# Kernel tuning notes

Measured on AMD Instinct MI355X. Metric: run time of the kernel, lower is better.

Reference implementation:

```python
import jax, jax.numpy as jnp
import numpy as np

B, H, W, D, K = 32, 64, 64, 128, 1024

def setup_inputs() -> dict:
    key = jax.random.key(0)
    k1, k2 = jax.random.split(key)
    inputs = jax.random.normal(k1, (B, H, W, D), dtype=jnp.float32)
    embedding = jax.random.normal(k2, (D, K), dtype=jnp.float32)  # codebook, column per code
    return {"inputs": inputs, "embedding": embedding}

def reference(inputs, embedding):
    D_ = embedding.shape[0]
    x = inputs.reshape(-1, D_)                                  # [N, D]
    dist = (jnp.sum(x * x, axis=-1, keepdims=True)
            - 2.0 * (x @ embedding)
            + jnp.sum(embedding * embedding, axis=0, keepdims=True))  # [N, K]
    idx = jnp.argmax(-dist, axis=1).reshape(inputs.shape[:-1])  # [B, H, W]
    return embedding.T[idx]                                     # [B, H, W, D]
```

## Files before the change

### kernel.cpp

```cpp
#include <hip/hip_runtime.h>

#define KC 1024
#define DD 128
#define NT_COUNT (KC / 16)

typedef short bf16x8 __attribute__((ext_vector_type(8)));
typedef float f32x4  __attribute__((ext_vector_type(4)));

#define AS1 __attribute__((address_space(1)))
#define AS3 __attribute__((address_space(3)))

static __device__ __forceinline__ unsigned short f2bf(float f) {
    unsigned u = __float_as_uint(f);
    unsigned r = (u + 0x7fffu + ((u >> 16) & 1u)) >> 16;
    return (unsigned short)r;
}
static __device__ __forceinline__ float bf2f(unsigned short h) {
    return __uint_as_float(((unsigned)h) << 16);
}
static __device__ __forceinline__ void gl_lds16(const void* g, void* l) {
    __builtin_amdgcn_global_load_lds((const AS1 void*)g, (AS3 void*)l, 16, 0, 0);
}
static __device__ __forceinline__ void gl_lds4(const void* g, void* l) {
    __builtin_amdgcn_global_load_lds((const AS1 void*)g, (AS3 void*)l, 4, 0, 0);
}

__global__ __launch_bounds__(256) void vq_prep(const float* __restrict__ E,
                                               float* __restrict__ e2h,
                                               float* __restrict__ ET,
                                               unsigned short* __restrict__ Bpk) {
    __shared__ float T[16 * 129];
    const int nt  = blockIdx.x;
    const int tid = threadIdx.x;

    for (int i = tid; i < 16 * DD; i += 256) {
        int d  = i >> 4;
        int kk = i & 15;
        T[kk * 129 + d] = E[(size_t)d * KC + nt * 16 + kk];
    }
    __syncthreads();

    if (tid < 16) {
        float s = 0.f;
#pragma unroll 16
        for (int d = 0; d < DD; ++d) {
            float v = T[tid * 129 + d];
            s = fmaf(v, v, s);
        }
        e2h[nt * 16 + tid] = 512.0f - 0.5f * s;
    }

    for (int i = tid; i < 16 * DD; i += 256) {
        int kk = i >> 7;
        int d  = i & 127;
        ET[(size_t)(nt * 16 + kk) * DD + d] = T[kk * 129 + d];
    }

    {
        const int s    = tid >> 6;
        const int lane = tid & 63;
        const int kk   = lane & 15;
        const int d0   = s * 32 + (lane >> 4) * 8;
        bf16x8 hi, lo;
#pragma unroll
        for (int j = 0; j < 8; ++j) {
            float v = T[kk * 129 + d0 + j];
            unsigned short h = f2bf(v);
            hi[j] = (short)h;
            lo[j] = (short)f2bf(v - bf2f(h));
        }
        char* base = (char*)Bpk + (size_t)nt * 8192 + s * 1024 + lane * 16;
        *(bf16x8*)(base)        = hi;
        *(bf16x8*)(base + 4096) = lo;
    }
}

__global__ __launch_bounds__(64, 3) void vq_main(const float* __restrict__ X,
                                                 const float* __restrict__ e2h,
                                                 const float* __restrict__ ET,
                                                 const unsigned short* __restrict__ Bpk,
                                                 float* __restrict__ Out) {
    __shared__ __align__(16) char lds[16896];
    int*    s_k1  = (int*)(lds);
    int*    s_k2  = (int*)(lds + 128);
    int*    s_win = (int*)(lds + 256);
    double* s_d   = (double*)(lds + 384);

    const int lane  = threadIdx.x;
    const int quad  = lane >> 4;
    const int n16   = lane & 15;
    const int wrow0 = blockIdx.x * 32;

    bf16x8 ahi[2][4], alo[2][4];
#pragma unroll
    for (int t = 0; t < 2; ++t) {
#pragma unroll
        for (int s = 0; s < 4; ++s) {
            const int row = wrow0 + t * 16 + n16;
            const int d0  = s * 32 + quad * 8;
            const float4 p = *(const float4*)(X + (size_t)row * DD + d0);
            const float4 q = *(const float4*)(X + (size_t)row * DD + d0 + 4);
            float v[8] = {p.x, p.y, p.z, p.w, q.x, q.y, q.z, q.w};
#pragma unroll
            for (int j = 0; j < 8; ++j) {
                unsigned short h = f2bf(v[j]);
                ahi[t][s][j] = (short)h;
                alo[t][s][j] = (short)f2bf(v[j] - bf2f(h));
            }
        }
    }

    float p1[2][4], p2[2][4];
#pragma unroll
    for (int t = 0; t < 2; ++t)
#pragma unroll
        for (int r = 0; r < 4; ++r) { p1[t][r] = 0.0f; p2[t][r] = 0.0f; }

    const char* gB = (const char*)Bpk + (size_t)lane * 16;

    auto stage = [&](int nt, int buf) {
        const char* g = gB + (size_t)nt * 8192;
        char* l = lds + buf * 8192;
#pragma unroll
        for (int c = 0; c < 8; ++c)
            gl_lds16(g + c * 1024, l + c * 1024);
        gl_lds4(e2h + nt * 16 + n16, lds + 16384 + buf * 256);
    };

    stage(0, 0);

    for (int nt = 0; nt < NT_COUNT; ++nt) {
        const int cur = nt & 1;
        if (nt + 1 < NT_COUNT) {
            stage(nt + 1, cur ^ 1);
            __builtin_amdgcn_s_waitcnt(3961);
        } else {
            __builtin_amdgcn_s_waitcnt(3952);
        }
        __builtin_amdgcn_sched_barrier(0);

        const char* l = lds + cur * 8192;
        const bf16x8 bh0 = *(const bf16x8*)(l + 0 * 1024 + lane * 16);
        const bf16x8 bh1 = *(const bf16x8*)(l + 1 * 1024 + lane * 16);
        const bf16x8 bh2 = *(const bf16x8*)(l + 2 * 1024 + lane * 16);
        const bf16x8 bh3 = *(const bf16x8*)(l + 3 * 1024 + lane * 16);
        const bf16x8 bl0 = *(const bf16x8*)(l + 4 * 1024 + lane * 16);
        const bf16x8 bl1 = *(const bf16x8*)(l + 5 * 1024 + lane * 16);
        const bf16x8 bl2 = *(const bf16x8*)(l + 6 * 1024 + lane * 16);
        const bf16x8 bl3 = *(const bf16x8*)(l + 7 * 1024 + lane * 16);
        const float  ev  = *(const float*)(lds + 16384 + cur * 256 + lane * 4);
        const unsigned ntinv = (unsigned)(63 - nt);

#pragma unroll
        for (int t = 0; t < 2; ++t) {
            f32x4 acc = {ev, ev, ev, ev};
            acc = __builtin_amdgcn_mfma_f32_16x16x32_bf16(ahi[t][0], bh0, acc, 0, 0, 0);
            acc = __builtin_amdgcn_mfma_f32_16x16x32_bf16(ahi[t][1], bh1, acc, 0, 0, 0);
            acc = __builtin_amdgcn_mfma_f32_16x16x32_bf16(ahi[t][2], bh2, acc, 0, 0, 0);
            acc = __builtin_amdgcn_mfma_f32_16x16x32_bf16(ahi[t][3], bh3, acc, 0, 0, 0);
            acc = __builtin_amdgcn_mfma_f32_16x16x32_bf16(alo[t][0], bh0, acc, 0, 0, 0);
            acc = __builtin_amdgcn_mfma_f32_16x16x32_bf16(alo[t][1], bh1, acc, 0, 0, 0);
            acc = __builtin_amdgcn_mfma_f32_16x16x32_bf16(alo[t][2], bh2, acc, 0, 0, 0);
            acc = __builtin_amdgcn_mfma_f32_16x16x32_bf16(alo[t][3], bh3, acc, 0, 0, 0);
            acc = __builtin_amdgcn_mfma_f32_16x16x32_bf16(ahi[t][0], bl0, acc, 0, 0, 0);
            acc = __builtin_amdgcn_mfma_f32_16x16x32_bf16(ahi[t][1], bl1, acc, 0, 0, 0);
            acc = __builtin_amdgcn_mfma_f32_16x16x32_bf16(ahi[t][2], bl2, acc, 0, 0, 0);
            acc = __builtin_amdgcn_mfma_f32_16x16x32_bf16(ahi[t][3], bl3, acc, 0, 0, 0);
#pragma unroll
            for (int r = 0; r < 4; ++r) {
                float v = __uint_as_float((__float_as_uint(acc[r]) & ~63u) | ntinv);
                float lo = fminf(p1[t][r], v);
                p1[t][r] = fmaxf(p1[t][r], v);
                p2[t][r] = fmaxf(p2[t][r], lo);
            }
        }
    }
    __syncthreads();

#pragma unroll
    for (int t = 0; t < 2; ++t) {
#pragma unroll
        for (int r = 0; r < 4; ++r) {
            unsigned u1 = __float_as_uint(p1[t][r]);
            unsigned u2 = __float_as_uint(p2[t][r]);
            int k1 = (int)(63u - (u1 & 63u)) * 16 + n16;
            int k2 = (int)(63u - (u2 & 63u)) * 16 + n16;
            unsigned long long q1 =
                ((unsigned long long)(u1 & ~63u) << 32) | (unsigned)(1023 - k1);
            unsigned long long q2 =
                ((unsigned long long)(u2 & ~63u) << 32) | (unsigned)(1023 - k2);
#pragma unroll
            for (int m = 1; m < 16; m <<= 1) {
                unsigned long long o1 = __shfl_xor(q1, m, 64);
                unsigned long long o2 = __shfl_xor(q2, m, 64);
                unsigned long long lo = q1 < o1 ? q1 : o1;
                q1 = q1 > o1 ? q1 : o1;
                unsigned long long hi2 = q2 > o2 ? q2 : o2;
                q2 = lo > hi2 ? lo : hi2;
            }
            if (n16 == 0) {
                int row = t * 16 + quad * 4 + r;
                s_k1[row] = 1023 - (int)(q1 & 1023u);
                s_k2[row] = 1023 - (int)(q2 & 1023u);
            }
        }
    }
    __syncthreads();

    {
        const int row = lane >> 1;
        const int k   = (lane & 1) ? s_k2[row] : s_k1[row];
        const float* __restrict__ xrow = X + (size_t)(wrow0 + row) * DD;
        const float* __restrict__ erow = ET + (size_t)k * DD;
        double dot = 0.0, ee = 0.0;
#pragma unroll 8
        for (int d = 0; d < DD; ++d) {
            double xv = (double)xrow[d];
            double evd = (double)erow[d];
            dot = fma(xv, evd, dot);
            ee  = fma(evd, evd, ee);
        }
        s_d[lane] = ee - 2.0 * dot;
    }
    __syncthreads();
    if (lane < 32) {
        double d1 = s_d[2 * lane];
        double d2 = s_d[2 * lane + 1];
        int kk1 = s_k1[lane], kk2 = s_k2[lane];
        s_win[lane] = (d2 < d1 || (d2 == d1 && kk2 < kk1)) ? kk2 : kk1;
    }
    __syncthreads();

    for (int i = lane; i < 32 * (DD / 4); i += 64) {
        const int row = i >> 5;
        const int d4  = i & 31;
        const float4 v = *(const float4*)(ET + (size_t)s_win[row] * DD + d4 * 4);
        *(float4*)(Out + (size_t)(wrow0 + row) * DD + d4 * 4) = v;
    }
}

extern "C" void kernel_launch(void* const* d_in, const int* in_sizes, int n_in,
                              void* d_out, int out_size, void* d_ws, size_t ws_size,
                              hipStream_t stream) {
    const float* X = (const float*)d_in[0];
    const float* E = (const float*)d_in[1];
    float* Out = (float*)d_out;

    float* e2h = (float*)d_ws;
    float* ET  = e2h + KC;
    unsigned short* Bpk = (unsigned short*)(ET + (size_t)KC * DD);

    const int N = in_sizes[0] / DD;

    hipLaunchKernelGGL(vq_prep, dim3(NT_COUNT), dim3(256), 0, stream, E, e2h, ET, Bpk);
    hipLaunchKernelGGL(vq_main, dim3(N / 32), dim3(64), 0, stream,
                       X, e2h, ET, Bpk, Out);
}
```

Before: 249.0 us.

## Double rows per wave to halve codebook LDS traffic and unroll pipeline by two

Each single-wave block now handles 64 rows (4 MFMA row tiles) instead of 32, so every staged codebook tile is reused across twice as many rows. This halves the total codebook global-to-LDS traffic and the number of blocks. The double-buffered loop is manually unrolled by two with fixed buffer offsets, and the exact fp64 rerank now has one lane per row checking both candidates. The cost is roughly double the register use for A fragments and accumulators, occupancy hint lowered from 3 to 2, and fewer blocks for load balance.

```diff
diff --git a/kernel.cpp b/kernel.cpp
--- a/kernel.cpp
+++ b/kernel.cpp
@@ -3,6 +3,7 @@
 #define KC 1024
 #define DD 128
 #define NT_COUNT (KC / 16)
+#define RPB 64
 
 typedef short bf16x8 __attribute__((ext_vector_type(8)));
 typedef float f32x4  __attribute__((ext_vector_type(4)));
@@ -75,25 +76,26 @@
     }
 }
 
-__global__ __launch_bounds__(64, 3) void vq_main(const float* __restrict__ X,
+__global__ __launch_bounds__(64, 2) void vq_main(const float* __restrict__ X,
                                                  const float* __restrict__ e2h,
                                                  const float* __restrict__ ET,
                                                  const unsigned short* __restrict__ Bpk,
                                                  float* __restrict__ Out) {
-    __shared__ __align__(16) char lds[16896];
-    int*    s_k1  = (int*)(lds);
-    int*    s_k2  = (int*)(lds + 128);
-    int*    s_win = (int*)(lds + 256);
-    double* s_d   = (double*)(lds + 384);
+    __shared__ __align__(16) char lds[2 * 8448];
+    int* s_k1  = (int*)(lds);
+    int* s_k2  = (int*)(lds + 256);
+    int* s_win = (int*)(lds + 512);
 
     const int lane  = threadIdx.x;
     const int quad  = lane >> 4;
     const int n16   = lane & 15;
-    const int wrow0 = blockIdx.x * 32;
-
-    bf16x8 ahi[2][4], alo[2][4];
-#pragma unroll
-    for (int t = 0; t < 2; ++t) {
+    const int wrow0 = blockIdx.x * RPB;
+    const int lidx16 = lane * 16;
+    const int lidx4  = lane * 4;
+
+    bf16x8 ahi[4][4], alo[4][4];
+#pragma unroll
+    for (int t = 0; t < 4; ++t) {
 #pragma unroll
         for (int s = 0; s < 4; ++s) {
             const int row = wrow0 + t * 16 + n16;
@@ -110,75 +112,79 @@
         }
     }
 
-    float p1[2][4], p2[2][4];
-#pragma unroll
-    for (int t = 0; t < 2; ++t)
+    float p1[4][4], p2[4][4];
+#pragma unroll
+    for (int t = 0; t < 4; ++t)
 #pragma unroll
         for (int r = 0; r < 4; ++r) { p1[t][r] = 0.0f; p2[t][r] = 0.0f; }
 
-    const char* gB = (const char*)Bpk + (size_t)lane * 16;
-
-    auto stage = [&](int nt, int buf) {
-        const char* g = gB + (size_t)nt * 8192;
-        char* l = lds + buf * 8192;
-#pragma unroll
-        for (int c = 0; c < 8; ++c)
-            gl_lds16(g + c * 1024, l + c * 1024);
-        gl_lds4(e2h + nt * 16 + n16, lds + 16384 + buf * 256);
-    };
-
-    stage(0, 0);
-
-    for (int nt = 0; nt < NT_COUNT; ++nt) {
-        const int cur = nt & 1;
-        if (nt + 1 < NT_COUNT) {
-            stage(nt + 1, cur ^ 1);
+#define STAGE(NT, BOFF)                                                          \
+    do {                                                                         \
+        const char* g = (const char*)Bpk + (size_t)(NT) * 8192;                  \
+        _Pragma("unroll")                                                        \
+        for (int c = 0; c < 8; ++c)                                              \
+            gl_lds16(g + c * 1024 + lidx16, lds + (BOFF) + c * 1024);            \
+        gl_lds4(e2h + (NT) * 16 + n16, lds + (BOFF) + 8192);                     \
+    } while (0)
+
+#define TILE(NT, BOFF)                                                           \
+    do {                                                                         \
+        const char* l = lds + (BOFF);                                            \
+        const bf16x8 bh0 = *(const bf16x8*)(l + 0 * 1024 + lidx16);              \
+        const bf16x8 bh1 = *(const bf16x8*)(l + 1 * 1024 + lidx16);              \
+        const bf16x8 bh2 = *(const bf16x8*)(l + 2 * 1024 + lidx16);              \
+        const bf16x8 bh3 = *(const bf16x8*)(l + 3 * 1024 + lidx16);              \
+        const bf16x8 bl0 = *(const bf16x8*)(l + 4 * 1024 + lidx16);              \
+        const bf16x8 bl1 = *(const bf16x8*)(l + 5 * 1024 + lidx16);              \
+        const bf16x8 bl2 = *(const bf16x8*)(l + 6 * 1024 + lidx16);              \
+        const bf16x8 bl3 = *(const bf16x8*)(l + 7 * 1024 + lidx16);              \
+        const float  ev  = *(const float*)(l + 8192 + lidx4);                    \
+        const unsigned ntinv = (unsigned)(63 - (NT));                            \
+        _Pragma("unroll")                                                        \
+        for (int t = 0; t < 4; ++t) {                                            \
+            f32x4 acc = {ev, ev, ev, ev};                                        \
+            acc = __builtin_amdgcn_mfma_f32_16x16x32_bf16(ahi[t][0], bh0, acc, 0, 0, 0); \
+            acc = __builtin_amdgcn_mfma_f32_16x16x32_bf16(ahi[t][1], bh1, acc, 0, 0, 0); \
+            acc = __builtin_amdgcn_mfma_f32_16x16x32_bf16(ahi[t][2], bh2, acc, 0, 0, 0); \
+            acc = __builtin_amdgcn_mfma_f32_16x16x32_bf16(ahi[t][3], bh3, acc, 0, 0, 0); \
+            acc = __builtin_amdgcn_mfma_f32_16x16x32_bf16(alo[t][0], bh0, acc, 0, 0, 0); \
+            acc = __builtin_amdgcn_mfma_f32_16x16x32_bf16(alo[t][1], bh1, acc, 0, 0, 0); \
+            acc = __builtin_amdgcn_mfma_f32_16x16x32_bf16(alo[t][2], bh2, acc, 0, 0, 0); \
+            acc = __builtin_amdgcn_mfma_f32_16x16x32_bf16(alo[t][3], bh3, acc, 0, 0, 0); \
+            acc = __builtin_amdgcn_mfma_f32_16x16x32_bf16(ahi[t][0], bl0, acc, 0, 0, 0); \
+            acc = __builtin_amdgcn_mfma_f32_16x16x32_bf16(ahi[t][1], bl1, acc, 0, 0, 0); \
+            acc = __builtin_amdgcn_mfma_f32_16x16x32_bf16(ahi[t][2], bl2, acc, 0, 0, 0); \
+            acc = __builtin_amdgcn_mfma_f32_16x16x32_bf16(ahi[t][3], bl3, acc, 0, 0, 0); \
+            _Pragma("unroll")                                                    \
+            for (int r = 0; r < 4; ++r) {                                        \
+                float v = __uint_as_float((__float_as_uint(acc[r]) & ~63u) | ntinv); \
+                float lo = fminf(p1[t][r], v);                                   \
+                p1[t][r] = fmaxf(p1[t][r], v);                                   \
+                p2[t][r] = fmaxf(p2[t][r], lo);                                  \
+            }                                                                    \
+        }                                                                        \
+    } while (0)
+
+    STAGE(0, 0);
+    for (int nt = 0; nt < NT_COUNT; nt += 2) {
+        STAGE(nt + 1, 8448);
+        __builtin_amdgcn_s_waitcnt(3961);
+        __builtin_amdgcn_sched_barrier(0);
+        TILE(nt, 0);
+        if (nt + 2 < NT_COUNT) {
+            STAGE(nt + 2, 0);
             __builtin_amdgcn_s_waitcnt(3961);
         } else {
             __builtin_amdgcn_s_waitcnt(3952);
         }
         __builtin_amdgcn_sched_barrier(0);
-
-        const char* l = lds + cur * 8192;
-        const bf16x8 bh0 = *(const bf16x8*)(l + 0 * 1024 + lane * 16);
-        const bf16x8 bh1 = *(const bf16x8*)(l + 1 * 1024 + lane * 16);
-        const bf16x8 bh2 = *(const bf16x8*)(l + 2 * 1024 + lane * 16);
-        const bf16x8 bh3 = *(const bf16x8*)(l + 3 * 1024 + lane * 16);
-        const bf16x8 bl0 = *(const bf16x8*)(l + 4 * 1024 + lane * 16);
-        const bf16x8 bl1 = *(const bf16x8*)(l + 5 * 1024 + lane * 16);
-        const bf16x8 bl2 = *(const bf16x8*)(l + 6 * 1024 + lane * 16);
-        const bf16x8 bl3 = *(const bf16x8*)(l + 7 * 1024 + lane * 16);
-        const float  ev  = *(const float*)(lds + 16384 + cur * 256 + lane * 4);
-        const unsigned ntinv = (unsigned)(63 - nt);
-
-#pragma unroll
-        for (int t = 0; t < 2; ++t) {
-            f32x4 acc = {ev, ev, ev, ev};
-            acc = __builtin_amdgcn_mfma_f32_16x16x32_bf16(ahi[t][0], bh0, acc, 0, 0, 0);
-            acc = __builtin_amdgcn_mfma_f32_16x16x32_bf16(ahi[t][1], bh1, acc, 0, 0, 0);
-            acc = __builtin_amdgcn_mfma_f32_16x16x32_bf16(ahi[t][2], bh2, acc, 0, 0, 0);
-            acc = __builtin_amdgcn_mfma_f32_16x16x32_bf16(ahi[t][3], bh3, acc, 0, 0, 0);
-            acc = __builtin_amdgcn_mfma_f32_16x16x32_bf16(alo[t][0], bh0, acc, 0, 0, 0);
-            acc = __builtin_amdgcn_mfma_f32_16x16x32_bf16(alo[t][1], bh1, acc, 0, 0, 0);
-            acc = __builtin_amdgcn_mfma_f32_16x16x32_bf16(alo[t][2], bh2, acc, 0, 0, 0);
-            acc = __builtin_amdgcn_mfma_f32_16x16x32_bf16(alo[t][3], bh3, acc, 0, 0, 0);
-            acc = __builtin_amdgcn_mfma_f32_16x16x32_bf16(ahi[t][0], bl0, acc, 0, 0, 0);
-            acc = __builtin_amdgcn_mfma_f32_16x16x32_bf16(ahi[t][1], bl1, acc, 0, 0, 0);
-            acc = __builtin_amdgcn_mfma_f32_16x16x32_bf16(ahi[t][2], bl2, acc, 0, 0, 0);
-            acc = __builtin_amdgcn_mfma_f32_16x16x32_bf16(ahi[t][3], bl3, acc, 0, 0, 0);
-#pragma unroll
-            for (int r = 0; r < 4; ++r) {
-                float v = __uint_as_float((__float_as_uint(acc[r]) & ~63u) | ntinv);
-                float lo = fminf(p1[t][r], v);
-                p1[t][r] = fmaxf(p1[t][r], v);
-                p2[t][r] = fmaxf(p2[t][r], lo);
-            }
-        }
-    }
-    __syncthreads();
-
-#pragma unroll
-    for (int t = 0; t < 2; ++t) {
+        TILE(nt + 1, 8448);
+    }
+#undef STAGE
+#undef TILE
+
+#pragma unroll
+    for (int t = 0; t < 4; ++t) {
 #pragma unroll
         for (int r = 0; r < 4; ++r) {
             unsigned u1 = __float_as_uint(p1[t][r]);
@@ -208,30 +214,29 @@
     __syncthreads();
 
     {
-        const int row = lane >> 1;
-        const int k   = (lane & 1) ? s_k2[row] : s_k1[row];
-        const float* __restrict__ xrow = X + (size_t)(wrow0 + row) * DD;
-        const float* __restrict__ erow = ET + (size_t)k * DD;
-        double dot = 0.0, ee = 0.0;
-#pragma unroll 8
+        const int k1 = s_k1[lane];
+        const int k2 = s_k2[lane];
+        const float* __restrict__ xrow = X + (size_t)(wrow0 + lane) * DD;
+        const float* __restrict__ e1 = ET + (size_t)k1 * DD;
+        const float* __restrict__ e2p = ET + (size_t)k2 * DD;
+        double dot1 = 0.0, ee1 = 0.0, dot2 = 0.0, ee2 = 0.0;
+#pragma unroll 4
         for (int d = 0; d < DD; ++d) {
             double xv = (double)xrow[d];
-            double evd = (double)erow[d];
-            dot = fma(xv, evd, dot);
-            ee  = fma(evd, evd, ee);
-        }
-        s_d[lane] = ee - 2.0 * dot;
+            double v1 = (double)e1[d];
+            double v2 = (double)e2p[d];
+            dot1 = fma(xv, v1, dot1);
+            ee1  = fma(v1, v1, ee1);
+            dot2 = fma(xv, v2, dot2);
+            ee2  = fma(v2, v2, ee2);
+        }
+        double d1 = ee1 - 2.0 * dot1;
+        double d2 = ee2 - 2.0 * dot2;
+        s_win[lane] = (d2 < d1 || (d2 == d1 && k2 < k1)) ? k2 : k1;
     }
     __syncthreads();
-    if (lane < 32) {
-        double d1 = s_d[2 * lane];
-        double d2 = s_d[2 * lane + 1];
-        int kk1 = s_k1[lane], kk2 = s_k2[lane];
-        s_win[lane] = (d2 < d1 || (d2 == d1 && kk2 < kk1)) ? kk2 : kk1;
-    }
-    __syncthreads();
-
-    for (int i = lane; i < 32 * (DD / 4); i += 64) {
+
+    for (int i = lane; i < RPB * (DD / 4); i += 64) {
         const int row = i >> 5;
         const int d4  = i & 31;
         const float4 v = *(const float4*)(ET + (size_t)s_win[row] * DD + d4 * 4);
@@ -253,6 +258,6 @@
     const int N = in_sizes[0] / DD;
 
     hipLaunchKernelGGL(vq_prep, dim3(NT_COUNT), dim3(256), 0, stream, E, e2h, ET, Bpk);
-    hipLaunchKernelGGL(vq_main, dim3(N / 32), dim3(64), 0, stream,
+    hipLaunchKernelGGL(vq_main, dim3(N / RPB), dim3(64), 0, stream,
                        X, e2h, ET, Bpk, Out);
 }
```

Result: faster. 234.9 us (-5.6%).
